# Optimization experiments

Hardware: AMD Instinct MI355X
Metric: run time of the kernel (lower is better)

## Reference

```python
import jax, jax.numpy as jnp
import numpy as np
import math

B, S, D, H = 2, 2048, 1024, 16
DH = D // H
PHI = (1 + math.sqrt(5)) / 2

def _carrier_phases(n_heads):
    # DimensionalHeadManager: 7 rungs with weights 1/phi^i, base phases k*pi/7,
    # per-rung heads spread uniformly around the circle.
    base = [k * math.pi / 7 for k in range(7)]
    raw_w = [1.0 / PHI ** i for i in range(7)]
    tw = sum(raw_w)
    alloc = [max(1, round(n_heads * w / tw)) for w in raw_w]
    while sum(alloc) > n_heads:
        alloc[alloc.index(max(alloc))] -= 1
    while sum(alloc) < n_heads:
        alloc[alloc.index(max(alloc))] += 1
    phases = []
    for r, c in enumerate(alloc):
        for j in range(c):
            phases.append(base[r] + 2 * math.pi / max(c, 1) * j)
    return np.array(phases, dtype=np.float32)

def setup_inputs() -> dict:
    key = jax.random.key(0)
    ks = jax.random.split(key, 8)
    x = jax.random.normal(ks[0], (B, S, D), dtype=jnp.float32)
    input_phase = jax.random.uniform(ks[1], (B, S), dtype=jnp.float32) * (2 * math.pi)
    sc = 1.0 / math.sqrt(D)
    Wq = jax.random.normal(ks[2], (D, D), dtype=jnp.float32) * sc
    Wk = jax.random.normal(ks[3], (D, D), dtype=jnp.float32) * sc
    Wv = jax.random.normal(ks[4], (D, D), dtype=jnp.float32) * sc
    Wo = jax.random.normal(ks[5], (D, D), dtype=jnp.float32) * sc
    gamma = jnp.ones((D,), dtype=jnp.float32)
    beta = jnp.zeros((D,), dtype=jnp.float32)
    # per-head fractal compression exponents > 1 (sub-linear for |x|<1)
    exponents = 1.0 + 0.5 * jax.random.uniform(ks[6], (H,), dtype=jnp.float32)
    carrier_phases = jnp.asarray(_carrier_phases(H))
    balance = jnp.asarray(0.5, dtype=jnp.float32)  # BALANCE
    return {"x": x, "input_phase": input_phase, "Wq": Wq, "Wk": Wk, "Wv": Wv,
            "Wo": Wo, "gamma": gamma, "beta": beta, "exponents": exponents,
            "carrier_phases": carrier_phases, "balance": balance}

def _layernorm(x, gamma, beta, eps=1e-5):
    mu = jnp.mean(x, axis=-1, keepdims=True)
    var = jnp.var(x, axis=-1, keepdims=True)
    return (x - mu) * jax.lax.rsqrt(var + eps) * gamma + beta

def _fractal_compress(kv, exps):
    # sign-preserving power-law compression, per-head exponent
    sign = jnp.sign(kv)
    mag = jnp.maximum(jnp.abs(kv), 1e-8)
    return sign * mag ** exps  # exps broadcast (1,H,1,1)

def reference(x, input_phase, Wq, Wk, Wv, Wo, gamma, beta, exponents,
              carrier_phases, balance):
    h = _layernorm(x, gamma, beta)
    def split_heads(t):
        return t.reshape(B, S, H, DH).transpose(0, 2, 1, 3)  # (B,H,S,dh)
    q = split_heads(h @ Wq)
    k = split_heads(h @ Wk)
    v = split_heads(h @ Wv)
    exps = exponents.reshape(1, H, 1, 1)
    k_c = _fractal_compress(k, exps)
    v_c = _fractal_compress(v, exps)
    # per-head carrier resonance: (B,S,H) in [0,1]
    T = jnp.cos((input_phase[:, :, None] - carrier_phases[None, None, :]) / 2.0) ** 2
    Th = T.transpose(0, 2, 1)  # (B,H,S)
    # balance temperature tau = clip(1/(2*balance), 0.1, 10)
    tau = jnp.clip(1.0 / (2.0 * balance + 1e-8), 0.1, 10.0)
    scores = jnp.einsum('bhqd,bhkd->bhqk', q, k_c) / math.sqrt(DH)
    # phase modulation: key-side resonance enters scores in log-space
    scores = scores + jnp.log(Th[:, :, None, :] + 1e-6)
    causal = jnp.tril(jnp.ones((S, S), dtype=bool))
    scores = jnp.where(causal[None, None], scores, jnp.float32(-1e9))
    attn = jax.nn.softmax(scores / tau, axis=-1)
    out = jnp.einsum('bhqk,bhkd->bhqd', attn, v_c)
    # query-side resonance gates the per-head output
    out = out * Th[:, :, :, None]
    out = out.transpose(0, 2, 1, 3).reshape(B, S, D)
    return x + out @ Wo
```

## Files before the change

kernel.cpp:

```cpp
#include <hip/hip_runtime.h>
#include <math.h>

namespace {
constexpr int B = 2, S = 2048, D = 1024, H = 16, DH = 64;
constexpr int BH = B * H;
constexpr int BS = B * S;
constexpr size_t MAT = (size_t)BS * D;
constexpr int QT = S / 64;
}

typedef __attribute__((ext_vector_type(8))) short s16x8;
typedef __attribute__((ext_vector_type(4))) short s16x4;
typedef __attribute__((ext_vector_type(4))) float f32x4;

__device__ inline unsigned short f2bf(float f) {
  union { float f; unsigned u; } c; c.f = f;
  unsigned r = c.u + 0x7fffu + ((c.u >> 16) & 1u);
  return (unsigned short)(r >> 16);
}
__device__ inline short f2bft(float f) {
  union { float f; unsigned u; } c; c.f = f;
  return (short)((c.u + 0x8000u) >> 16);
}
__device__ inline float bf2f(short s) {
  union { unsigned u; float f; } c;
  c.u = ((unsigned)(unsigned short)s) << 16;
  return c.f;
}
__device__ inline void gld16(const unsigned short* g, unsigned short* l) {
  __builtin_amdgcn_global_load_lds(
      (const __attribute__((address_space(1))) unsigned int*)g,
      (__attribute__((address_space(3))) unsigned int*)l, 16, 0, 0);
}

__global__ __launch_bounds__(256) void k_prep(
    const float* __restrict__ x, const float* __restrict__ gamma,
    const float* __restrict__ beta, unsigned short* __restrict__ h,
    const float* __restrict__ phase, const float* __restrict__ cp,
    const float* __restrict__ bal, float* __restrict__ Th,
    float* __restrict__ Lt, const float* __restrict__ W0,
    const float* __restrict__ W1, const float* __restrict__ W2,
    const float* __restrict__ W3, unsigned short* __restrict__ T0,
    unsigned short* __restrict__ T1, unsigned short* __restrict__ T2,
    unsigned short* __restrict__ T3) {
  __shared__ float shbuf[32 * 33];
  int id = blockIdx.x;
  int t = threadIdx.x;
  if (id < 4096) {
    int z = id & 3;
    int bx = ((id >> 2) & 31) * 32;
    int by = (id >> 7) * 32;
    const float* W = (z == 0) ? W0 : (z == 1) ? W1 : (z == 2) ? W2 : W3;
    unsigned short* T = (z == 0) ? T0 : (z == 1) ? T1 : (z == 2) ? T2 : T3;
    int tc = t & 31, tr = t >> 5;
    float(*tile)[33] = (float(*)[33])shbuf;
#pragma unroll
    for (int i = 0; i < 4; i++)
      tile[tr + 8 * i][tc] = W[(size_t)(by + tr + 8 * i) * D + bx + tc];
    __syncthreads();
#pragma unroll
    for (int i = 0; i < 4; i++)
      T[(size_t)(bx + tr + 8 * i) * D + by + tc] = f2bf(tile[tc][tr + 8 * i]);
  } else if (id < 8192) {
    int row = id - 4096;
    float* red = shbuf;
    const float* xr = x + (size_t)row * D;
    float v[4];
    float s = 0.f;
#pragma unroll
    for (int i = 0; i < 4; i++) {
      v[i] = xr[t + 256 * i];
      s += v[i];
    }
    red[t] = s;
    __syncthreads();
    for (int off = 128; off > 0; off >>= 1) {
      if (t < off) red[t] += red[t + off];
      __syncthreads();
    }
    float mu = red[0] * (1.0f / D);
    __syncthreads();
    float s2 = 0.f;
#pragma unroll
    for (int i = 0; i < 4; i++) {
      float d0 = v[i] - mu;
      s2 += d0 * d0;
    }
    red[t] = s2;
    __syncthreads();
    for (int off = 128; off > 0; off >>= 1) {
      if (t < off) red[t] += red[t + off];
      __syncthreads();
    }
    float r = rsqrtf(red[0] * (1.0f / D) + 1e-5f);
    unsigned short* hr = h + (size_t)row * D;
#pragma unroll
    for (int i = 0; i < 4; i++) {
      int c = t + 256 * i;
      hr[c] = f2bf((v[i] - mu) * r * gamma[c] + beta[c]);
    }
  } else {
    int idx = (id - 8192) * 256 + t;
    int s = idx & (S - 1);
    int bh = idx >> 11;
    int hh = bh & (H - 1);
    int b = bh >> 4;
    float tau = fminf(fmaxf(1.0f / (2.0f * bal[0] + 1e-8f), 0.1f), 10.0f);
    float c = cosf((phase[b * S + s] - cp[hh]) * 0.5f);
    float T = c * c;
    Th[idx] = T;
    Lt[idx] = __log2f(T + 1e-6f) * (1.0f / tau);
  }
}

#define MFMA_GEMM_LOOP_TBUF(AP, BP)                                           \
  do {                                                                        \
    gld16(AP, &As[0][chunkA][0]);                                             \
    gld16(AP + (size_t)16 * D, &As[0][chunkA + 16][0]);                       \
    gld16(BP, &Bs[0][chunkA][0]);                                             \
    gld16(BP + (size_t)16 * D, &Bs[0][chunkA + 16][0]);                       \
    gld16(AP + 32, &As[1][chunkA][0]);                                        \
    gld16(AP + (size_t)16 * D + 32, &As[1][chunkA + 16][0]);                  \
    gld16(BP + 32, &Bs[1][chunkA][0]);                                        \
    gld16(BP + (size_t)16 * D + 32, &Bs[1][chunkA + 16][0]);                  \
    int cur = 0;                                                              \
    for (int k0 = 0; k0 < D; k0 += 32) {                                      \
      if (k0 + 32 < D)                                                        \
        asm volatile("s_waitcnt vmcnt(4)" ::: "memory");                      \
      else                                                                    \
        asm volatile("s_waitcnt vmcnt(0)" ::: "memory");                      \
      asm volatile("s_barrier" ::: "memory");                                 \
      if (k0 + 64 < D) {                                                      \
        int nxt = (cur >= 1) ? cur - 1 : 2;                    \
        gld16(AP + k0 + 64, &As[nxt][chunkA][0]);                             \
        gld16(AP + (size_t)16 * D + k0 + 64, &As[nxt][chunkA + 16][0]);       \
        gld16(BP + k0 + 64, &Bs[nxt][chunkA][0]);                             \
        gld16(BP + (size_t)16 * D + k0 + 64, &Bs[nxt][chunkA + 16][0]);       \
      }                                                                       \
      s16x8 af[4], bf[4];                                                     \
      _Pragma("unroll") for (int i = 0; i < 4; i++) {                         \
        af[i] = *(const s16x8*)&As[cur][wm + i * 16 + lane16][quad * 8];      \
        bf[i] = *(const s16x8*)&Bs[cur][wn + i * 16 + lane16][quad * 8];      \
      }                                                                       \
      _Pragma("unroll") for (int i = 0; i < 4; i++)                           \
          _Pragma("unroll") for (int j = 0; j < 4; j++) acc[i][j] =           \
          __builtin_amdgcn_mfma_f32_16x16x32_bf16(af[i], bf[j], acc[i][j],    \
                                                  0, 0, 0);                   \
      cur = (cur == 2) ? 0 : cur + 1;                                         \
    }                                                                         \
  } while (0)

__global__ __launch_bounds__(512) void k_gemm_qkvv(
    const unsigned short* __restrict__ hm, const unsigned short* __restrict__ Wq,
    const unsigned short* __restrict__ Wk, const unsigned short* __restrict__ Wv,
    const float* __restrict__ exps, unsigned short* __restrict__ q,
    unsigned short* __restrict__ kc, unsigned short* __restrict__ vt) {
  __shared__ __align__(16) unsigned short As[3][256][32];
  __shared__ __align__(16) unsigned short Bs[3][128][32];
  int id = blockIdx.x;
  int xcd = id & 7;
  int g = id >> 3;
  int z = g >> 4;
  int w = g & 15;
  const unsigned short *Ap, *Bp;
  int tileM, tileN;
  if (z < 2) {
    Ap = hm; Bp = (z == 0) ? Wq : Wk;
    tileM = ((xcd >> 1) * 4 + (w >> 2)) * 256;
    tileN = ((xcd & 1) * 4 + (w & 3)) * 128;
  } else {
    Ap = Wv; Bp = hm;
    tileM = ((xcd & 1) * 2 + (w >> 3)) * 256;
    tileN = ((xcd >> 1) * 8 + (w & 7)) * 128;
  }
  int t = threadIdx.x;
  int wave = t >> 6, lane = t & 63, lane16 = lane & 15, quad = lane >> 4;
  int wm = (wave >> 1) * 64;
  int wn = (wave & 1) * 64;
  int chunkA = wave * 32;
  int chunkB = wave * 16;
  int srow = (lane >> 2), scol = (lane & 3) * 8;
  const unsigned short* aptr = Ap + (size_t)(tileM + chunkA + srow) * D + scol;
  const unsigned short* bptr = Bp + (size_t)(tileN + chunkB + srow) * D + scol;
  f32x4 acc[4][4] = {};
  gld16(aptr, &As[0][chunkA][0]);
  gld16(aptr + (size_t)16 * D, &As[0][chunkA + 16][0]);
  gld16(bptr, &Bs[0][chunkB][0]);
  gld16(aptr + 32, &As[1][chunkA][0]);
  gld16(aptr + (size_t)16 * D + 32, &As[1][chunkA + 16][0]);
  gld16(bptr + 32, &Bs[1][chunkB][0]);
  int cur = 0;
  for (int k0 = 0; k0 < D; k0 += 32) {
    if (k0 + 32 < D)
      asm volatile("s_waitcnt vmcnt(3)" ::: "memory");
    else
      asm volatile("s_waitcnt vmcnt(0)" ::: "memory");
    asm volatile("s_barrier" ::: "memory");
    if (k0 + 64 < D) {
      int nxt = (cur >= 1) ? cur - 1 : 2;
      gld16(aptr + k0 + 64, &As[nxt][chunkA][0]);
      gld16(aptr + (size_t)16 * D + k0 + 64, &As[nxt][chunkA + 16][0]);
      gld16(bptr + k0 + 64, &Bs[nxt][chunkB][0]);
    }
    s16x8 af[4], bf[4];
#pragma unroll
    for (int i = 0; i < 4; i++) {
      af[i] = *(const s16x8*)&As[cur][wm + i * 16 + lane16][quad * 8];
      bf[i] = *(const s16x8*)&Bs[cur][wn + i * 16 + lane16][quad * 8];
    }
#pragma unroll
    for (int i = 0; i < 4; i++)
#pragma unroll
      for (int j = 0; j < 4; j++)
        acc[i][j] = __builtin_amdgcn_mfma_f32_16x16x32_bf16(af[i], bf[j],
                                                            acc[i][j], 0, 0, 0);
    cur = (cur == 2) ? 0 : cur + 1;
  }
  if (z < 2) {
    unsigned short* __restrict__ outp = (z == 0) ? q : kc;
    float e0 = exps[tileN >> 6];
    float e1 = exps[(tileN >> 6) + 1];
#pragma unroll
    for (int i = 0; i < 4; i++) {
#pragma unroll
      for (int r = 0; r < 4; r++) {
        int row = tileM + wm + i * 16 + quad * 4 + r;
        int b = row >> 11, s = row & (S - 1);
#pragma unroll
        for (int j = 0; j < 4; j++) {
          int cloc = wn + j * 16 + lane16;
          int head = (tileN + cloc) >> 6;
          int dh = cloc & 63;
          float val = acc[i][j][r];
          if (z != 0) {
            float e = (cloc >> 6) ? e1 : e0;
            float sgn = (val > 0.f) ? 1.f : ((val < 0.f) ? -1.f : 0.f);
            float mg = fmaxf(fabsf(val), 1e-8f);
            val = sgn * exp2f(e * __log2f(mg));
          }
          outp[((size_t)(b * H + head) * S + s) * DH + dh] = f2bf(val);
        }
      }
    }
  } else {
#pragma unroll
    for (int i = 0; i < 4; i++) {
#pragma unroll
      for (int r = 0; r < 4; r++) {
        int m = tileM + wm + i * 16 + quad * 4 + r;
        int head = m >> 6, dh = m & 63;
        float e = exps[head];
#pragma unroll
        for (int j = 0; j < 4; j++) {
          int n = tileN + wn + j * 16 + lane16;
          int b = n >> 11, s = n & (S - 1);
          float val = acc[i][j][r];
          float sgn = (val > 0.f) ? 1.f : ((val < 0.f) ? -1.f : 0.f);
          float mg = fmaxf(fabsf(val), 1e-8f);
          val = sgn * exp2f(e * __log2f(mg));
          vt[((size_t)(b * H + head) * DH + dh) * S + s] = f2bf(val);
        }
      }
    }
  }
}

__global__ __launch_bounds__(256) void k_gemm_out_mfma(
    const unsigned short* __restrict__ am, const unsigned short* __restrict__ Wt,
    const float* __restrict__ x, float* __restrict__ outp) {
  __shared__ __align__(16) unsigned short As[3][128][32];
  __shared__ __align__(16) unsigned short Bs[3][128][32];
  int id = blockIdx.x;
  int xcd = id & 7;
  int inner = id >> 3;
  int tileM = ((xcd >> 1) * 8 + (inner >> 2)) * 128;
  int tileN = ((xcd & 1) * 4 + (inner & 3)) * 128;
  int t = threadIdx.x;
  int wave = t >> 6, lane = t & 63, lane16 = lane & 15, quad = lane >> 4;
  int wm = (wave >> 1) * 64, wn = (wave & 1) * 64;
  int chunkA = wave * 32;
  int srow = (lane >> 2), scol = (lane & 3) * 8;
  const unsigned short* aptr = am + (size_t)(tileM + chunkA + srow) * D + scol;
  const unsigned short* bptr = Wt + (size_t)(tileN + chunkA + srow) * D + scol;
  f32x4 acc[4][4] = {};
  MFMA_GEMM_LOOP_TBUF(aptr, bptr);
#pragma unroll
  for (int i = 0; i < 4; i++) {
#pragma unroll
    for (int r = 0; r < 4; r++) {
      int row = tileM + wm + i * 16 + quad * 4 + r;
      const float* xr = x + (size_t)row * D;
      float* orow = outp + (size_t)row * D;
#pragma unroll
      for (int j = 0; j < 4; j++) {
        int col = tileN + wn + j * 16 + lane16;
        orow[col] = xr[col] + acc[i][j][r];
      }
    }
  }
}

__global__ __launch_bounds__(256) void k_attn_mfma(
    const unsigned short* __restrict__ q, const unsigned short* __restrict__ kc,
    const unsigned short* __restrict__ vt, const float* __restrict__ Th,
    const float* __restrict__ Lt, const float* __restrict__ bal,
    unsigned short* __restrict__ ao) {
  __shared__ __align__(16) unsigned short Ks[2][64][64];
  __shared__ __align__(16) unsigned short Vs[2][64][64];
  __shared__ __align__(16) unsigned short Pt[4][16][72];
  __shared__ __align__(16) float Lts[2][64];
  int id = blockIdx.x;
  int bh = (id & 7) + 8 * ((id >> 3) & 3);
  int qt = QT - 1 - (id >> 5);
  int t = threadIdx.x;
  int wave = t >> 6, lane = t & 63;
  int lane16 = lane & 15, quad = lane >> 4;
  float tau = fminf(fmaxf(1.0f / (2.0f * bal[0] + 1e-8f), 0.1f), 10.0f);
  float c1 = 0.125f * (1.0f / tau) * 1.44269504f;
  const unsigned short* qb = q + (size_t)bh * S * DH;
  const unsigned short* kb = kc + (size_t)bh * S * DH;
  const unsigned short* vb = vt + (size_t)bh * DH * S;
  const float* Ltb = Lt + (size_t)bh * S;
  int b = bh >> 4, hh = bh & (H - 1);
  int cr = t >> 3, cc = (t & 7) * 8;
  int wsw = ((cr & 7) << 4);
  int wcol = (cc * 2) ^ wsw;
  s16x8 nk0, nk1, nv0, nv1;
  float4 nlt;
#define STAGE_LOAD(KT)                                                  \
  do {                                                                  \
    nk0 = *(const s16x8*)(kb + (size_t)((KT) * 64 + cr) * DH + cc);     \
    nk1 = *(const s16x8*)(kb + (size_t)((KT) * 64 + cr + 32) * DH + cc);\
    nv0 = *(const s16x8*)(vb + (size_t)cr * S + (KT) * 64 + cc);        \
    nv1 = *(const s16x8*)(vb + (size_t)(cr + 32) * S + (KT) * 64 + cc); \
    if (t < 16) nlt = ((const float4*)(Ltb + (KT) * 64))[t];            \
  } while (0)
#define STAGE_WRITE(BF)                                                 \
  do {                                                                  \
    *(s16x8*)((char*)&Ks[BF][cr][0] + wcol) = nk0;                      \
    *(s16x8*)((char*)&Ks[BF][cr + 32][0] + wcol) = nk1;                 \
    *(s16x8*)((char*)&Vs[BF][cr][0] + wcol) = nv0;                      \
    *(s16x8*)((char*)&Vs[BF][cr + 32][0] + wcol) = nv1;                 \
    if (t < 16) ((float4*)Lts[BF])[t] = nlt;                            \
  } while (0)
  int qbase = qt * 64 + wave * 16;
  s16x8 qa0, qa1;
  {
    s16x8 r0 = *(const s16x8*)(qb + (size_t)(qbase + lane16) * DH + quad * 8);
    s16x8 r1 =
        *(const s16x8*)(qb + (size_t)(qbase + lane16) * DH + 32 + quad * 8);
#pragma unroll
    for (int i = 0; i < 8; i++) {
      qa0[i] = f2bft(bf2f(r0[i]) * c1);
      qa1[i] = f2bft(bf2f(r1[i]) * c1);
    }
  }
  STAGE_LOAD(0);
  STAGE_WRITE(0);
  __syncthreads();
  f32x4 O[4] = {};
  float lacc = 0.f;
  int rsw = ((lane16 & 7) << 4);
  int rc0 = (quad * 16) ^ rsw;
  int rc1 = (64 + quad * 16) ^ rsw;
  for (int kt = 0; kt <= qt; kt++) {
    int cur = kt & 1;
    if (kt < qt) STAGE_LOAD(kt + 1);
    bool diag = (kt == qt);
#pragma unroll
    for (int jk = 0; jk < 4; jk++) {
      s16x8 ka0 = *(const s16x8*)((const char*)&Ks[cur][jk * 16 + lane16][0] + rc0);
      s16x8 ka1 = *(const s16x8*)((const char*)&Ks[cur][jk * 16 + lane16][0] + rc1);
      f32x4 st = {};
      st = __builtin_amdgcn_mfma_f32_16x16x32_bf16(ka0, qa0, st, 0, 0, 0);
      st = __builtin_amdgcn_mfma_f32_16x16x32_bf16(ka1, qa1, st, 0, 0, 0);
      float4 ltv = *(const float4*)&Lts[cur][jk * 16 + quad * 4];
      float lt4[4] = {ltv.x, ltv.y, ltv.z, ltv.w};
      s16x4 pk;
#pragma unroll
      for (int r = 0; r < 4; r++) {
        float vv = fminf(st[r] + lt4[r], 126.f);
        float p = exp2f(vv);
        if (diag)
          p = (jk * 16 + quad * 4 + r <= wave * 16 + lane16) ? p : 0.f;
        lacc += p;
        pk[r] = f2bft(p);
      }
      *(s16x4*)&Pt[wave][lane16][jk * 16 + quad * 4] = pk;
    }
    s16x8 pf0 = *(const s16x8*)&Pt[wave][lane16][quad * 8];
    s16x8 pf1 = *(const s16x8*)&Pt[wave][lane16][32 + quad * 8];
#pragma unroll
    for (int d = 0; d < 4; d++) {
      s16x8 av0 = *(const s16x8*)((const char*)&Vs[cur][d * 16 + lane16][0] + rc0);
      s16x8 av1 = *(const s16x8*)((const char*)&Vs[cur][d * 16 + lane16][0] + rc1);
      O[d] = __builtin_amdgcn_mfma_f32_16x16x32_bf16(av0, pf0, O[d], 0, 0, 0);
      O[d] = __builtin_amdgcn_mfma_f32_16x16x32_bf16(av1, pf1, O[d], 0, 0, 0);
    }
    if (kt < qt) STAGE_WRITE(cur ^ 1);
    __syncthreads();
  }
  lacc += __shfl_xor(lacc, 16, 64);
  lacc += __shfl_xor(lacc, 32, 64);
  int qg = qbase + lane16;
  float scl = Th[(size_t)bh * S + qg] / lacc;
  unsigned short* op = ao + (size_t)(b * S + qg) * D + hh * DH;
#pragma unroll
  for (int d = 0; d < 4; d++) {
    s16x4 pk;
#pragma unroll
    for (int r = 0; r < 4; r++) pk[r] = f2bft(O[d][r] * scl);
    *(s16x4*)(op + d * 16 + quad * 4) = pk;
  }
#undef STAGE_LOAD
#undef STAGE_WRITE
}

extern "C" void kernel_launch(void* const* d_in, const int* in_sizes, int n_in,
                              void* d_out, int out_size, void* d_ws,
                              size_t ws_size, hipStream_t stream) {
  const float* x = (const float*)d_in[0];
  const float* phase = (const float*)d_in[1];
  const float* Wq = (const float*)d_in[2];
  const float* Wk = (const float*)d_in[3];
  const float* Wv = (const float*)d_in[4];
  const float* Wo = (const float*)d_in[5];
  const float* gamma = (const float*)d_in[6];
  const float* beta = (const float*)d_in[7];
  const float* exps = (const float*)d_in[8];
  const float* cph = (const float*)d_in[9];
  const float* bal = (const float*)d_in[10];
  float* out = (float*)d_out;

  unsigned short* hbuf = (unsigned short*)d_ws;
  float* Thbuf = (float*)(hbuf + MAT);
  float* Ltbuf = Thbuf + (size_t)BH * S;
  unsigned short* qbuf = (unsigned short*)(Ltbuf + (size_t)BH * S);
  unsigned short* kbuf = qbuf + MAT;
  unsigned short* vtbuf = kbuf + MAT;
  unsigned short* aobuf = vtbuf + MAT;
  unsigned short* wq_t = aobuf + MAT;
  unsigned short* wk_t = wq_t + (size_t)D * D;
  unsigned short* wv_t = wk_t + (size_t)D * D;
  unsigned short* wo_t = wv_t + (size_t)D * D;

  hipLaunchKernelGGL(k_prep, dim3(8448), dim3(256), 0, stream, x, gamma, beta,
                     hbuf, phase, cph, bal, Thbuf, Ltbuf, Wq, Wk, Wv, Wo, wq_t,
                     wk_t, wv_t, wo_t);
  hipLaunchKernelGGL(k_gemm_qkvv, dim3(384), dim3(512), 0, stream, hbuf, wq_t,
                     wk_t, wv_t, exps, qbuf, kbuf, vtbuf);
  hipLaunchKernelGGL(k_attn_mfma, dim3(1024), dim3(256), 0, stream, qbuf,
                     kbuf, vtbuf, Thbuf, Ltbuf, bal, aobuf);
  hipLaunchKernelGGL(k_gemm_out_mfma, dim3(256), dim3(256), 0, stream, aobuf,
                     wo_t, x, out);
}
```

Baseline: 199.8 us.

## Software-pipeline attention loop: overlap PV of previous tile with QK softmax of current

The attention loop is restructured so each iteration runs the P·V MFMAs for tile kt-1 and the QK^T plus exp for tile kt. P is double-buffered and V is triple-buffered in shared memory so this skew works. The goal is to hide MFMA latency and the LDS round-trip of P behind independent work. The log-resonance bias is also folded into the MFMA accumulator init, which removes one add per element. The cost is more LDS per block, which may lower occupancy, plus a longer prologue and epilogue.

Result: slower. 212.2 us (+6.2%).

```diff
diff --git a/kernel.cpp b/kernel.cpp
--- a/kernel.cpp
+++ b/kernel.cpp
@@ -306,8 +306,8 @@
     const float* __restrict__ Lt, const float* __restrict__ bal,
     unsigned short* __restrict__ ao) {
   __shared__ __align__(16) unsigned short Ks[2][64][64];
-  __shared__ __align__(16) unsigned short Vs[2][64][64];
-  __shared__ __align__(16) unsigned short Pt[4][16][72];
+  __shared__ __align__(16) unsigned short Vs[3][64][64];
+  __shared__ __align__(16) unsigned short Pt[2][4][16][72];
   __shared__ __align__(16) float Lts[2][64];
   int id = blockIdx.x;
   int bh = (id & 7) + 8 * ((id >> 3) & 3);
@@ -335,13 +335,14 @@
     nv1 = *(const s16x8*)(vb + (size_t)(cr + 32) * S + (KT) * 64 + cc); \
     if (t < 16) nlt = ((const float4*)(Ltb + (KT) * 64))[t];            \
   } while (0)
-#define STAGE_WRITE(BF)                                                 \
+#define STAGE_WRITE(KT_)                                                \
   do {                                                                  \
-    *(s16x8*)((char*)&Ks[BF][cr][0] + wcol) = nk0;                      \
-    *(s16x8*)((char*)&Ks[BF][cr + 32][0] + wcol) = nk1;                 \
-    *(s16x8*)((char*)&Vs[BF][cr][0] + wcol) = nv0;                      \
-    *(s16x8*)((char*)&Vs[BF][cr + 32][0] + wcol) = nv1;                 \
-    if (t < 16) ((float4*)Lts[BF])[t] = nlt;                            \
+    int kb_ = (KT_) & 1, vb_ = (KT_) % 3;                               \
+    *(s16x8*)((char*)&Ks[kb_][cr][0] + wcol) = nk0;                     \
+    *(s16x8*)((char*)&Ks[kb_][cr + 32][0] + wcol) = nk1;                \
+    *(s16x8*)((char*)&Vs[vb_][cr][0] + wcol) = nv0;                     \
+    *(s16x8*)((char*)&Vs[vb_][cr + 32][0] + wcol) = nv1;                \
+    if (t < 16) ((float4*)Lts[kb_])[t] = nlt;                           \
   } while (0)
   int qbase = qt * 64 + wave * 16;
   s16x8 qa0, qa1;
@@ -355,51 +356,64 @@
       qa1[i] = f2bft(bf2f(r1[i]) * c1);
     }
   }
-  STAGE_LOAD(0);
-  STAGE_WRITE(0);
-  __syncthreads();
   f32x4 O[4] = {};
   float lacc = 0.f;
   int rsw = ((lane16 & 7) << 4);
   int rc0 = (quad * 16) ^ rsw;
   int rc1 = (64 + quad * 16) ^ rsw;
-  for (int kt = 0; kt <= qt; kt++) {
-    int cur = kt & 1;
+#define QKSM(KT)                                                        \
+  do {                                                                  \
+    int kbuf_ = (KT) & 1;                                               \
+    bool diag_ = ((KT) == qt);                                          \
+    _Pragma("unroll") for (int jk = 0; jk < 4; jk++) {                  \
+      s16x8 ka0 = *(const s16x8*)((const char*)&Ks[kbuf_][jk * 16 +     \
+                                  lane16][0] + rc0);                    \
+      s16x8 ka1 = *(const s16x8*)((const char*)&Ks[kbuf_][jk * 16 +     \
+                                  lane16][0] + rc1);                    \
+      float4 ltv = *(const float4*)&Lts[kbuf_][jk * 16 + quad * 4];     \
+      f32x4 st = {ltv.x, ltv.y, ltv.z, ltv.w};                          \
+      st = __builtin_amdgcn_mfma_f32_16x16x32_bf16(ka0, qa0, st, 0, 0, 0); \
+      st = __builtin_amdgcn_mfma_f32_16x16x32_bf16(ka1, qa1, st, 0, 0, 0); \
+      s16x4 pk;                                                         \
+      _Pragma("unroll") for (int r = 0; r < 4; r++) {                   \
+        float p = exp2f(fminf(st[r], 126.f));                           \
+        if (diag_)                                                      \
+          p = (jk * 16 + quad * 4 + r <= wave * 16 + lane16) ? p : 0.f; \
+        lacc += p;                                                      \
+        pk[r] = f2bft(p);                                               \
+      }                                                                 \
+      *(s16x4*)&Pt[kbuf_][wave][lane16][jk * 16 + quad * 4] = pk;       \
+    }                                                                   \
+  } while (0)
+#define PVSTEP(KT)                                                      \
+  do {                                                                  \
+    int pb_ = (KT) & 1, vbuf_ = (KT) % 3;                               \
+    s16x8 pf0 = *(const s16x8*)&Pt[pb_][wave][lane16][quad * 8];        \
+    s16x8 pf1 = *(const s16x8*)&Pt[pb_][wave][lane16][32 + quad * 8];   \
+    _Pragma("unroll") for (int d = 0; d < 4; d++) {                     \
+      s16x8 av0 = *(const s16x8*)((const char*)&Vs[vbuf_][d * 16 +      \
+                                  lane16][0] + rc0);                    \
+      s16x8 av1 = *(const s16x8*)((const char*)&Vs[vbuf_][d * 16 +      \
+                                  lane16][0] + rc1);                    \
+      O[d] = __builtin_amdgcn_mfma_f32_16x16x32_bf16(av0, pf0, O[d], 0, 0, 0); \
+      O[d] = __builtin_amdgcn_mfma_f32_16x16x32_bf16(av1, pf1, O[d], 0, 0, 0); \
+    }                                                                   \
+  } while (0)
+  STAGE_LOAD(0);
+  STAGE_WRITE(0);
+  __syncthreads();
+  if (qt >= 1) STAGE_LOAD(1);
+  QKSM(0);
+  if (qt >= 1) STAGE_WRITE(1);
+  __syncthreads();
+  for (int kt = 1; kt <= qt; kt++) {
     if (kt < qt) STAGE_LOAD(kt + 1);
-    bool diag = (kt == qt);
-#pragma unroll
-    for (int jk = 0; jk < 4; jk++) {
-      s16x8 ka0 = *(const s16x8*)((const char*)&Ks[cur][jk * 16 + lane16][0] + rc0);
-      s16x8 ka1 = *(const s16x8*)((const char*)&Ks[cur][jk * 16 + lane16][0] + rc1);
-      f32x4 st = {};
-      st = __builtin_amdgcn_mfma_f32_16x16x32_bf16(ka0, qa0, st, 0, 0, 0);
-      st = __builtin_amdgcn_mfma_f32_16x16x32_bf16(ka1, qa1, st, 0, 0, 0);
-      float4 ltv = *(const float4*)&Lts[cur][jk * 16 + quad * 4];
-      float lt4[4] = {ltv.x, ltv.y, ltv.z, ltv.w};
-      s16x4 pk;
-#pragma unroll
-      for (int r = 0; r < 4; r++) {
-        float vv = fminf(st[r] + lt4[r], 126.f);
-        float p = exp2f(vv);
-        if (diag)
-          p = (jk * 16 + quad * 4 + r <= wave * 16 + lane16) ? p : 0.f;
-        lacc += p;
-        pk[r] = f2bft(p);
-      }
-      *(s16x4*)&Pt[wave][lane16][jk * 16 + quad * 4] = pk;
-    }
-    s16x8 pf0 = *(const s16x8*)&Pt[wave][lane16][quad * 8];
-    s16x8 pf1 = *(const s16x8*)&Pt[wave][lane16][32 + quad * 8];
-#pragma unroll
-    for (int d = 0; d < 4; d++) {
-      s16x8 av0 = *(const s16x8*)((const char*)&Vs[cur][d * 16 + lane16][0] + rc0);
-      s16x8 av1 = *(const s16x8*)((const char*)&Vs[cur][d * 16 + lane16][0] + rc1);
-      O[d] = __builtin_amdgcn_mfma_f32_16x16x32_bf16(av0, pf0, O[d], 0, 0, 0);
-      O[d] = __builtin_amdgcn_mfma_f32_16x16x32_bf16(av1, pf1, O[d], 0, 0, 0);
-    }
-    if (kt < qt) STAGE_WRITE(cur ^ 1);
+    PVSTEP(kt - 1);
+    QKSM(kt);
+    if (kt < qt) STAGE_WRITE(kt + 1);
     __syncthreads();
   }
+  PVSTEP(qt);
   lacc += __shfl_xor(lacc, 16, 64);
   lacc += __shfl_xor(lacc, 32, 64);
   int qg = qbase + lane16;
@@ -414,6 +428,8 @@
   }
 #undef STAGE_LOAD
 #undef STAGE_WRITE
+#undef QKSM
+#undef PVSTEP
 }
 
 extern "C" void kernel_launch(void* const* d_in, const int* in_sizes, int n_in,
```
